# Kernel optimization log

Measured on AMD Instinct MI355X. Metric: run time of the kernel, lower is better.

The kernel has to match this reference:

```python
import jax, jax.numpy as jnp
import numpy as np

# Dims: B=batch, C=n_car, N=n_node, E=embed_dim, H=n_heads
B, C, N, E = 64, 8, 512, 512
H = 8
CLIP = 10.0


def setup_inputs() -> dict:
    key = jax.random.key(0)
    ks = jax.random.split(key, 12)
    s = 1.0 / np.sqrt(E)
    mask = jax.random.bernoulli(ks[10], 0.3, (B, C, 1, N))
    mask = mask.at[..., 0].set(False)  # ensure at least one unmasked node per (b,c)
    return {
        "node_embeddings": jax.random.normal(ks[0], (B, N, E), jnp.float32),
        "graph_embedding": jax.random.normal(ks[1], (B, E), jnp.float32),
        "step_context": jax.random.normal(ks[2], (B, C, 1, E + 2), jnp.float32),
        "mask": mask,
        "Wk1": jax.random.normal(ks[3], (E, E), jnp.float32) * s,
        "Wv": jax.random.normal(ks[4], (E, E), jnp.float32) * s,
        "Wk2": jax.random.normal(ks[5], (E, E), jnp.float32) * s,
        "Wq_fixed": jax.random.normal(ks[6], (E, E), jnp.float32) * s,
        "Wout": jax.random.normal(ks[7], (E, E), jnp.float32) * s,
        "Wq_step": jax.random.normal(ks[8], (E, E + 2), jnp.float32) * s,
        "v": jax.random.uniform(ks[9], (E,), jnp.float32, -s, s),
    }


def reference(node_embeddings, graph_embedding, step_context, mask,
              Wk1, Wv, Wk2, Wq_fixed, Wout, Wq_step, v):
    dh = E // H
    neg = jnp.asarray(-1e9, node_embeddings.dtype)

    # compute_static: projections (torch Linear: x @ W.T). K/V/Q_fixed are
    # broadcast over the car dim instead of materialized via .repeat (same math).
    Q_fixed = (graph_embedding @ Wq_fixed.T)[:, None, None, :]  # [B,1,1,E]
    K1 = node_embeddings @ Wk1.T                                 # [B,N,E]
    V = node_embeddings @ Wv.T                                   # [B,N,E]
    K2 = node_embeddings @ Wk2.T                                 # [B,N,E]

    # compute_dynamic
    Q_step = step_context @ Wq_step.T                            # [B,C,1,E]
    Q1 = Q_fixed + Q_step                                        # [B,C,1,E]

    # MHA (need_W=False): split heads, masked scaled dot-product, merge heads.
    qh = Q1.reshape(B, C, H, dh)                                 # q-len 1 squeezed
    kh = K1.reshape(B, N, H, dh)
    vh = V.reshape(B, N, H, dh)
    scores = jnp.einsum('bchd,bnhd->bchn', qh, kh) * (1.0 / np.sqrt(dh))
    m = mask[:, :, 0, :][:, :, None, :]                          # [B,C,1,N]
    scores = jnp.where(m, neg, scores)
    attn = jax.nn.softmax(scores, axis=-1)
    heads = jnp.einsum('bchn,bnhd->bchd', attn, vh).reshape(B, C, E)
    Q3 = heads @ Wout.T                                          # [B,C,E] (Q2.squeeze(2))

    # Pointer logits (SHA): u = tanh(Q_fixed+Q_step) @ v, repeated over E,
    # dotted with K2 => u_scalar * sum_e K2, then tanh-clipped and masked.
    u_scalar = jnp.einsum('bcqe,e->bcq', jnp.tanh(Q1), v)        # [B,C,1]
    k2sum = K2.sum(-1)                                           # [B,N]
    raw = u_scalar * k2sum[:, None, :]                           # [B,C,N]
    logits = CLIP * jnp.tanh(raw * (1.0 / np.sqrt(E)))
    logits = jnp.where(mask[:, :, 0, :], neg, logits)
    logits = logits.reshape(B, C * N)                            # view(batch, -1)
    return logits, Q3
```

## Files before the change

kernel.cpp:

```cpp
#include <hip/hip_runtime.h>


typedef _Float16 f16x8 __attribute__((ext_vector_type(8)));
typedef float f32x4 __attribute__((ext_vector_type(4)));

__device__ __forceinline__ void async16(const void* g, void* l) {
  __builtin_amdgcn_global_load_lds(
      (const __attribute__((address_space(1))) unsigned int*)g,
      (__attribute__((address_space(3))) unsigned int*)l, 16, 0, 0);
}

__global__ __launch_bounds__(256) void prep_w(const float* __restrict__ Wk1,
                                              const float* __restrict__ Wv,
                                              const float* __restrict__ Wk2,
                                              _Float16* __restrict__ W1h,
                                              _Float16* __restrict__ W2h,
                                              float* __restrict__ colsum) {
  const int bid = blockIdx.x;
  if (bid < 16) {
    const int tx = threadIdx.x & 31, ty = threadIdx.x >> 5;
    const int col = bid * 32 + tx;
    float s = 0.f;
#pragma unroll 4
    for (int e = ty * 64; e < ty * 64 + 64; ++e) s += Wk2[e * 512 + col];
    __shared__ float red[8][32];
    red[ty][tx] = s;
    __syncthreads();
    if (ty == 0) {
      float t = 0.f;
#pragma unroll
      for (int g = 0; g < 8; ++g) t += red[g][tx];
      colsum[col] = t;
    }
  } else {
    const int cb = bid - 16;
    const float* src = (cb < 128) ? Wk1 : Wv;
    _Float16* dst = (cb < 128) ? W1h : W2h;
    const size_t off = (size_t)(cb & 127) * 2048 + threadIdx.x * 8;
    float4 a = *(const float4*)(src + off);
    float4 b = *(const float4*)(src + off + 4);
    union { _Float16 h[8]; uint4 u; } pk;
    pk.h[0] = (_Float16)a.x; pk.h[1] = (_Float16)a.y;
    pk.h[2] = (_Float16)a.z; pk.h[3] = (_Float16)a.w;
    pk.h[4] = (_Float16)b.x; pk.h[5] = (_Float16)b.y;
    pk.h[6] = (_Float16)b.z; pk.h[7] = (_Float16)b.w;
    *(uint4*)(dst + off) = pk.u;
  }
}

__global__ __launch_bounds__(256) void q1_mfma_kernel(
    const float* __restrict__ ge, const float* __restrict__ sc,
    const float* __restrict__ Wqf, const float* __restrict__ Wqs,
    float* __restrict__ Q1) {
  const int mb = blockIdx.x, nb = blockIdx.y, ks = blockIdx.z;
  const int tid = threadIdx.x;
  const int lane = tid & 63, wave = tid >> 6;
  const int wm = (wave >> 1) * 32, wn = (wave & 1) * 32;

  __shared__ __align__(16) _Float16 As[64][40];
  __shared__ __align__(16) _Float16 Ws[64][40];

  f32x4 acc[2][2] = {};
  const int qd = (lane >> 4) * 8, rr = lane & 15;

  for (int kt = 0; kt < 9; ++kt) {
    const int kb = ks * 288 + kt * 32;
#pragma unroll
    for (int f0 = 0; f0 < 2; ++f0) {
      int f = tid + f0 * 256;
      int r = f >> 3, c4 = (f & 7) * 4;
      int m = mb * 64 + r;
      int e = nb * 64 + r;
#pragma unroll
      for (int j = 0; j < 4; ++j) {
        int k = kb + c4 + j;
        float a = 0.f, w = 0.f;
        if (k < 512) {
          a = ge[(m >> 3) * 512 + k];
          w = Wqf[(size_t)e * 512 + k];
        } else if (k < 1026) {
          a = sc[(size_t)m * 514 + (k - 512)];
          w = Wqs[(size_t)e * 514 + (k - 512)];
        }
        As[r][c4 + j] = (_Float16)a;
        Ws[r][c4 + j] = (_Float16)w;
      }
    }
    __syncthreads();
    f16x8 af[2], bfr[2];
#pragma unroll
    for (int mi = 0; mi < 2; ++mi) af[mi] = *(const f16x8*)&As[wm + mi * 16 + rr][qd];
#pragma unroll
    for (int ni = 0; ni < 2; ++ni) bfr[ni] = *(const f16x8*)&Ws[wn + ni * 16 + rr][qd];
#pragma unroll
    for (int mi = 0; mi < 2; ++mi)
#pragma unroll
      for (int ni = 0; ni < 2; ++ni)
        acc[mi][ni] =
            __builtin_amdgcn_mfma_f32_16x16x32_f16(af[mi], bfr[ni], acc[mi][ni], 0, 0, 0);
    __syncthreads();
  }

  const int col = lane & 15, rq = (lane >> 4) * 4;
#pragma unroll
  for (int mi = 0; mi < 2; ++mi)
#pragma unroll
    for (int ni = 0; ni < 2; ++ni)
#pragma unroll
      for (int r = 0; r < 4; ++r) {
        int m = mb * 64 + wm + mi * 16 + rq + r;
        int e = nb * 64 + wn + ni * 16 + col;
        atomicAdd(&Q1[(size_t)m * 512 + e], acc[mi][ni][r]);
      }
}

__global__ __launch_bounds__(256, 2) void gemm_kv(
    const float* __restrict__ A, const _Float16* __restrict__ W1,
    const _Float16* __restrict__ W2, const float* __restrict__ colsum,
    _Float16* __restrict__ K1, _Float16* __restrict__ Vt,
    float* __restrict__ k2sum) {
  const int nb = blockIdx.x;
  const int mb = blockIdx.y;
  const int tid = threadIdx.x, lane = tid & 63, wave = tid >> 6;
  const int wm = (wave >> 1) * 64, wn = (wave & 1) * 64;
  const int row0 = mb * 128, col0 = nb * 128;
  const int b = mb >> 2;

  __shared__ __align__(16) float Afs[128 * 64];
  __shared__ __align__(16) _Float16 Wbuf[2][128 * 64];

  f32x4 acc1[4][4] = {}, acc2[4][4] = {};
  float k2p = 0.f;
  const int q = lane >> 4, rr = lane & 15;
  const int wlr = lane >> 3, wlc = lane & 7;
  const int cswz = wlc ^ wlr;

  for (int kt = 0; kt < 8; ++kt) {
    const int kbase = kt * 64;
#pragma unroll
    for (int j = 0; j < 4; ++j) {
      int r = wave * 32 + j * 8 + wlr;
      int ldsrow = (wave * 32 + j * 8) * 64;
      size_t goff = (size_t)(col0 + r) * 512 + kbase + cswz * 8;
      async16(W1 + goff, &Wbuf[0][ldsrow]);
      async16(W2 + goff, &Wbuf[1][ldsrow]);
    }
#pragma unroll
    for (int j = 0; j < 8; ++j) {
      int r = wave * 32 + j * 4 + (lane >> 4);
      int cg = (lane & 15) ^ (r & 7);
      async16(A + (size_t)(row0 + r) * 512 + kbase + cg * 4,
              &Afs[(wave * 32 + j * 4) * 64]);
    }
    __syncthreads();
#pragma unroll
    for (int k0 = 0; k0 < 64; k0 += 32) {
      const int cb = (k0 >> 3) + q;
      const int ca = (k0 >> 2) + q * 2;
      f16x8 af[4], b1[4], b2[4];
#pragma unroll
      for (int mi = 0; mi < 4; ++mi) {
        int ra = wm + mi * 16 + rr;
        const float* base = &Afs[ra * 64];
        float4 lo = *(const float4*)(base + ((ca ^ (ra & 7)) * 4));
        float4 hi = *(const float4*)(base + (((ca + 1) ^ (ra & 7)) * 4));
        f16x8 v;
        v[0] = (_Float16)lo.x; v[1] = (_Float16)lo.y;
        v[2] = (_Float16)lo.z; v[3] = (_Float16)lo.w;
        v[4] = (_Float16)hi.x; v[5] = (_Float16)hi.y;
        v[6] = (_Float16)hi.z; v[7] = (_Float16)hi.w;
        af[mi] = v;
      }
#pragma unroll
      for (int ni = 0; ni < 4; ++ni) {
        int rw = wn + ni * 16 + rr;
        int slot = cb ^ (rw & 7);
        b1[ni] = *(const f16x8*)&Wbuf[0][rw * 64 + slot * 8];
        b2[ni] = *(const f16x8*)&Wbuf[1][rw * 64 + slot * 8];
      }
#pragma unroll
      for (int mi = 0; mi < 4; ++mi)
#pragma unroll
        for (int ni = 0; ni < 4; ++ni) {
          acc1[mi][ni] =
              __builtin_amdgcn_mfma_f32_16x16x32_f16(af[mi], b1[ni], acc1[mi][ni], 0, 0, 0);
          acc2[mi][ni] =
              __builtin_amdgcn_mfma_f32_16x16x32_f16(af[mi], b2[ni], acc2[mi][ni], 0, 0, 0);
        }
    }
    if (nb == 0) {
      int r = tid >> 1, cb0 = (tid & 1) * 8;
      const float* csp = colsum + kbase;
#pragma unroll
      for (int c = cb0; c < cb0 + 8; ++c) {
        int slot = c ^ (r & 7);
        float4 av = *(const float4*)&Afs[r * 64 + slot * 4];
        float4 cv = *(const float4*)(csp + c * 4);
        k2p += av.x * cv.x + av.y * cv.y + av.z * cv.z + av.w * cv.w;
      }
    }
    __syncthreads();
  }

  if (nb == 0) {
    k2p += __shfl_xor(k2p, 1, 64);
    if ((tid & 1) == 0) k2sum[row0 + (tid >> 1)] = k2p;
  }

  const int col = lane & 15, rq = (lane >> 4) * 4;
#pragma unroll
  for (int mi = 0; mi < 4; ++mi)
#pragma unroll
    for (int ni = 0; ni < 4; ++ni)
#pragma unroll
      for (int r = 0; r < 4; ++r) {
        size_t m = row0 + wm + mi * 16 + rq + r;
        size_t e = col0 + wn + ni * 16 + col;
        K1[m * 512 + e] = (_Float16)acc1[mi][ni][r];
      }

  _Float16* Vts = (_Float16*)&Afs[0];
#pragma unroll
  for (int mi = 0; mi < 4; ++mi)
#pragma unroll
    for (int ni = 0; ni < 4; ++ni) {
      int n0 = wm + mi * 16 + rq;
      int el = wn + ni * 16 + col;
      int cn = n0 >> 3, half = (n0 >> 2) & 1;
      int slot = cn ^ (el & 7);
      union { _Float16 h[4]; unsigned long long u; } pk;
#pragma unroll
      for (int r = 0; r < 4; ++r) pk.h[r] = (_Float16)acc2[mi][ni][r];
      *(unsigned long long*)&Vts[el * 128 + slot * 8 + half * 4] = pk.u;
    }
  __syncthreads();
  const int nbase = row0 & 511;
#pragma unroll
  for (int i = 0; i < 8; ++i) {
    int f = tid + i * 256;
    int el = f >> 4, c16 = f & 15;
    int slot = c16 ^ (el & 7);
    uint4 val = *(const uint4*)&Vts[el * 128 + slot * 8];
    *(uint4*)(Vt + (size_t)b * 262144 + (size_t)(col0 + el) * 512 + nbase + c16 * 8) = val;
  }
}

__global__ __launch_bounds__(256) void attn_kernel(
    const float* __restrict__ Q1, const _Float16* __restrict__ K1,
    const _Float16* __restrict__ Vt, const int* __restrict__ mask,
    float* __restrict__ heads) {
  const int bid = blockIdx.x;
  const int b = bid >> 3, h = bid & 7;
  const int tid = threadIdx.x, wave = tid >> 6, lane = tid & 63;
  const int q = lane >> 4, cl = lane & 15;

  __shared__ __align__(16) _Float16 kt[256 * 64];
  __shared__ __align__(16) _Float16 P[16][520];
  __shared__ float red[4][8];

  f16x8 af[2];
  {
    const float* qp = Q1 + (size_t)(b * 8 + (cl & 7)) * 512 + h * 64 + q * 8;
#pragma unroll
    for (int s = 0; s < 2; ++s) {
      float4 l0 = *(const float4*)(qp + s * 32);
      float4 l1 = *(const float4*)(qp + s * 32 + 4);
      af[s][0] = (_Float16)l0.x; af[s][1] = (_Float16)l0.y;
      af[s][2] = (_Float16)l0.z; af[s][3] = (_Float16)l0.w;
      af[s][4] = (_Float16)l1.x; af[s][5] = (_Float16)l1.y;
      af[s][6] = (_Float16)l1.z; af[s][7] = (_Float16)l1.w;
    }
  }

  f32x4 acc[8] = {};
  const _Float16* Kb = K1 + (size_t)b * 262144 + h * 64;
  for (int h2 = 0; h2 < 2; ++h2) {
#pragma unroll
    for (int j = 0; j < 8; ++j) {
      int r = wave * 64 + j * 8 + (lane >> 3);
      int cg = (lane & 7) ^ (r & 7);
      async16(Kb + (size_t)(h2 * 256 + r) * 512 + cg * 8, &kt[(wave * 64 + j * 8) * 64]);
    }
    __syncthreads();
#pragma unroll
    for (int tt = 0; tt < 4; ++tt) {
      int rn = wave * 64 + tt * 16 + cl;
#pragma unroll
      for (int s = 0; s < 2; ++s) {
        int slot = (s * 4 + q) ^ (cl & 7);
        f16x8 bf = *(const f16x8*)&kt[rn * 64 + slot * 8];
        acc[h2 * 4 + tt] =
            __builtin_amdgcn_mfma_f32_16x16x32_f16(af[s], bf, acc[h2 * 4 + tt], 0, 0, 0);
      }
    }
    __syncthreads();
  }

  const _Float16* Vb = Vt + (size_t)b * 262144 + (size_t)h * 64 * 512;
#pragma unroll
  for (int j = 0; j < 8; ++j) {
    int r = wave * 16 + j * 2 + (lane >> 5);
    int cg = (lane & 31) ^ (r & 7);
    async16(Vb + (size_t)r * 512 + cg * 8, &kt[(wave * 16 + j * 2) * 256]);
  }

  float gmax[4], rsum[4];
  if (q < 2) {
    float mx[4] = {-3e38f, -3e38f, -3e38f, -3e38f};
#pragma unroll
    for (int t = 0; t < 8; ++t) {
      int n = (t >> 2) * 256 + wave * 64 + (t & 3) * 16 + cl;
#pragma unroll
      for (int r = 0; r < 4; ++r) {
        int c = q * 4 + r;
        float x = mask[(size_t)(b * 8 + c) * 512 + n] ? -1e9f : acc[t][r] * 0.125f;
        acc[t][r] = x;
        mx[r] = fmaxf(mx[r], x);
      }
    }
#pragma unroll
    for (int off = 1; off < 16; off <<= 1)
#pragma unroll
      for (int r = 0; r < 4; ++r) mx[r] = fmaxf(mx[r], __shfl_xor(mx[r], off, 64));
    if (cl == 0)
#pragma unroll
      for (int r = 0; r < 4; ++r) red[wave][q * 4 + r] = mx[r];
  }
  __syncthreads();
  if (q < 2) {
#pragma unroll
    for (int r = 0; r < 4; ++r) {
      int c = q * 4 + r;
      gmax[r] = fmaxf(fmaxf(red[0][c], red[1][c]), fmaxf(red[2][c], red[3][c]));
    }
  }
  __syncthreads();
  if (q < 2) {
#pragma unroll
    for (int r = 0; r < 4; ++r) rsum[r] = 0.f;
#pragma unroll
    for (int t = 0; t < 8; ++t) {
      int n = (t >> 2) * 256 + wave * 64 + (t & 3) * 16 + cl;
#pragma unroll
      for (int r = 0; r < 4; ++r) {
        float e = __expf(acc[t][r] - gmax[r]);
        rsum[r] += e;
        P[q * 4 + r][n] = (_Float16)e;
      }
    }
#pragma unroll
    for (int off = 1; off < 16; off <<= 1)
#pragma unroll
      for (int r = 0; r < 4; ++r) rsum[r] += __shfl_xor(rsum[r], off, 64);
    if (cl == 0)
#pragma unroll
      for (int r = 0; r < 4; ++r) red[wave][q * 4 + r] = rsum[r];
  }
  __syncthreads();

  f32x4 pacc = {};
  const int rn = wave * 16 + cl;
#pragma unroll
  for (int sl = 0; sl < 8; ++sl) {
    int slot = (sl * 4 + q) ^ (cl & 7);
    f16x8 bf = *(const f16x8*)&kt[rn * 256 + slot * 8];
    f16x8 pa = *(const f16x8*)&P[cl][sl * 32 + q * 8];
    pacc = __builtin_amdgcn_mfma_f32_16x16x32_f16(pa, bf, pacc, 0, 0, 0);
  }
  __syncthreads();
#pragma unroll
  for (int j = 0; j < 8; ++j) {
    int r = wave * 16 + j * 2 + (lane >> 5);
    int cg = (lane & 31) ^ (r & 7);
    async16(Vb + (size_t)r * 512 + 256 + cg * 8, &kt[(wave * 16 + j * 2) * 256]);
  }
  __syncthreads();
#pragma unroll
  for (int sl = 0; sl < 8; ++sl) {
    int slot = (sl * 4 + q) ^ (cl & 7);
    f16x8 bf = *(const f16x8*)&kt[rn * 256 + slot * 8];
    f16x8 pa = *(const f16x8*)&P[cl][256 + sl * 32 + q * 8];
    pacc = __builtin_amdgcn_mfma_f32_16x16x32_f16(pa, bf, pacc, 0, 0, 0);
  }

  if (q < 2) {
#pragma unroll
    for (int r = 0; r < 4; ++r) {
      int c = q * 4 + r;
      float inv = 1.f / (red[0][c] + red[1][c] + red[2][c] + red[3][c]);
      heads[(size_t)(b * 8 + c) * 512 + h * 64 + wave * 16 + cl] = pacc[r] * inv;
    }
  }
}

__global__ __launch_bounds__(256) void gemm_out64(const float* __restrict__ A,
                                                  const float* __restrict__ W,
                                                  float* __restrict__ C) {
  const int mb = blockIdx.x, nb = blockIdx.y, ks = blockIdx.z;
  const int tid = threadIdx.x;
  const int lane = tid & 63, wave = tid >> 6;
  const int wm = (wave >> 1) * 32, wn = (wave & 1) * 32;

  __shared__ __align__(16) _Float16 As[64][40];
  __shared__ __align__(16) _Float16 Ws[64][40];

  f32x4 acc[2][2] = {};
  const int qd = (lane >> 4) * 8, rr = lane & 15;

  for (int kt = 0; kt < 8; ++kt) {
    const int kb = ks * 256 + kt * 32;
#pragma unroll
    for (int f0 = 0; f0 < 2; ++f0) {
      int f = tid + f0 * 256;
      int r = f >> 3, c4 = (f & 7) * 4;
      float4 a = *(const float4*)(A + (size_t)(mb * 64 + r) * 512 + kb + c4);
      float4 w = *(const float4*)(W + (size_t)(nb * 64 + r) * 512 + kb + c4);
      As[r][c4 + 0] = (_Float16)a.x; As[r][c4 + 1] = (_Float16)a.y;
      As[r][c4 + 2] = (_Float16)a.z; As[r][c4 + 3] = (_Float16)a.w;
      Ws[r][c4 + 0] = (_Float16)w.x; Ws[r][c4 + 1] = (_Float16)w.y;
      Ws[r][c4 + 2] = (_Float16)w.z; Ws[r][c4 + 3] = (_Float16)w.w;
    }
    __syncthreads();
    f16x8 af[2], bfr[2];
#pragma unroll
    for (int mi = 0; mi < 2; ++mi) af[mi] = *(const f16x8*)&As[wm + mi * 16 + rr][qd];
#pragma unroll
    for (int ni = 0; ni < 2; ++ni) bfr[ni] = *(const f16x8*)&Ws[wn + ni * 16 + rr][qd];
#pragma unroll
    for (int mi = 0; mi < 2; ++mi)
#pragma unroll
      for (int ni = 0; ni < 2; ++ni)
        acc[mi][ni] =
            __builtin_amdgcn_mfma_f32_16x16x32_f16(af[mi], bfr[ni], acc[mi][ni], 0, 0, 0);
    __syncthreads();
  }

  const int col = lane & 15, rq = (lane >> 4) * 4;
#pragma unroll
  for (int mi = 0; mi < 2; ++mi)
#pragma unroll
    for (int ni = 0; ni < 2; ++ni)
#pragma unroll
      for (int r = 0; r < 4; ++r) {
        int m = mb * 64 + wm + mi * 16 + rq + r;
        int e = nb * 64 + wn + ni * 16 + col;
        atomicAdd(&C[(size_t)m * 512 + e], acc[mi][ni][r]);
      }
}

__global__ __launch_bounds__(256) void logits_u_kernel(
    const float* __restrict__ Q1, const float* __restrict__ v,
    const float* __restrict__ k2s, const int* __restrict__ mask,
    float* __restrict__ out) {
  const int bc = blockIdx.x;
  const int b = bc >> 3;
  const int tid = threadIdx.x;
  const int wave = tid >> 6, lane = tid & 63;

  float p = tanhf(Q1[(size_t)bc * 512 + tid]) * v[tid] +
            tanhf(Q1[(size_t)bc * 512 + tid + 256]) * v[tid + 256];
#pragma unroll
  for (int off = 32; off; off >>= 1) p += __shfl_down(p, off, 64);
  __shared__ float red[4];
  __shared__ float su;
  if (lane == 0) red[wave] = p;
  __syncthreads();
  if (tid == 0) su = red[0] + red[1] + red[2] + red[3];
  __syncthreads();
  const float u = su;

#pragma unroll
  for (int i = 0; i < 2; ++i) {
    int n = tid + i * 256;
    int idx = bc * 512 + n;
    out[idx] = mask[idx] ? -1e9f
                         : 10.f * tanhf(u * k2s[b * 512 + n] * 0.04419417382415922f);
  }
}

extern "C" void kernel_launch(void* const* d_in, const int* in_sizes, int n_in,
                              void* d_out, int out_size, void* d_ws, size_t ws_size,
                              hipStream_t stream) {
  const float* ne = (const float*)d_in[0];
  const float* ge = (const float*)d_in[1];
  const float* sc = (const float*)d_in[2];
  const int* mask = (const int*)d_in[3];
  const float* Wk1 = (const float*)d_in[4];
  const float* Wv = (const float*)d_in[5];
  const float* Wk2 = (const float*)d_in[6];
  const float* Wqf = (const float*)d_in[7];
  const float* Wout = (const float*)d_in[8];
  const float* Wqs = (const float*)d_in[9];
  const float* v = (const float*)d_in[10];

  float* logits = (float*)d_out;
  float* q3 = (float*)d_out + 262144;

  char* ws = (char*)d_ws;
  _Float16* K1 = (_Float16*)(ws + 0);
  _Float16* Vt = (_Float16*)(ws + 33554432);
  float* Q1 = (float*)(ws + 67108864);
  float* heads = (float*)(ws + 68157440);
  float* k2sum = (float*)(ws + 69206016);
  float* colsum = (float*)(ws + 69337088);
  _Float16* W1h = (_Float16*)(ws + 69339136);
  _Float16* W2h = (_Float16*)(ws + 69863424);

  hipMemsetAsync(Q1, 0, 1048576, stream);
  hipMemsetAsync(q3, 0, 1048576, stream);
  prep_w<<<272, 256, 0, stream>>>(Wk1, Wv, Wk2, W1h, W2h, colsum);
  q1_mfma_kernel<<<dim3(8, 8, 4), 256, 0, stream>>>(ge, sc, Wqf, Wqs, Q1);
  gemm_kv<<<dim3(4, 256), 256, 0, stream>>>(ne, W1h, W2h, colsum, K1, Vt, k2sum);
  attn_kernel<<<512, 256, 0, stream>>>(Q1, K1, Vt, mask, heads);
  gemm_out64<<<dim3(8, 8, 2), 256, 0, stream>>>(heads, Wout, q3);
  logits_u_kernel<<<512, 256, 0, stream>>>(Q1, v, k2sum, mask, logits);
}
```

Before: 224.3 us.

## Double-buffer W tiles and prefetch A via registers with fp16 LDS staging

New measurement: 214.4 us. 1.05x faster.

```diff
diff --git a/kernel.cpp b/kernel.cpp
--- a/kernel.cpp
+++ b/kernel.cpp
@@ -126,57 +126,90 @@
   const int row0 = mb * 128, col0 = nb * 128;
   const int b = mb >> 2;
 
-  __shared__ __align__(16) float Afs[128 * 64];
-  __shared__ __align__(16) _Float16 Wbuf[2][128 * 64];
+  __shared__ __align__(16) _Float16 Ah[128 * 64];
+  __shared__ __align__(16) _Float16 Wb[2][2][128 * 64];
 
   f32x4 acc1[4][4] = {}, acc2[4][4] = {};
-  float k2p = 0.f;
+  float k2p[4] = {0.f, 0.f, 0.f, 0.f};
   const int q = lane >> 4, rr = lane & 15;
   const int wlr = lane >> 3, wlc = lane & 7;
   const int cswz = wlc ^ wlr;
 
-  for (int kt = 0; kt < 8; ++kt) {
+  const int ar0 = tid >> 3, ac = tid & 7;
+  const float* aptr = A + (size_t)(row0 + ar0) * 512 + ac * 8;
+  const int aslot = ac ^ (ar0 & 7);
+
+  float4 areg[4][2];
+
+  auto issue_a = [&](int kt) {
+#pragma unroll
+    for (int j = 0; j < 4; ++j) {
+      const float* gp = aptr + (size_t)j * 32 * 512 + kt * 64;
+      areg[j][0] = *(const float4*)gp;
+      areg[j][1] = *(const float4*)(gp + 4);
+    }
+  };
+  auto issue_w = [&](int kt, int buf) {
     const int kbase = kt * 64;
 #pragma unroll
     for (int j = 0; j < 4; ++j) {
       int r = wave * 32 + j * 8 + wlr;
       int ldsrow = (wave * 32 + j * 8) * 64;
       size_t goff = (size_t)(col0 + r) * 512 + kbase + cswz * 8;
-      async16(W1 + goff, &Wbuf[0][ldsrow]);
-      async16(W2 + goff, &Wbuf[1][ldsrow]);
-    }
-#pragma unroll
-    for (int j = 0; j < 8; ++j) {
-      int r = wave * 32 + j * 4 + (lane >> 4);
-      int cg = (lane & 15) ^ (r & 7);
-      async16(A + (size_t)(row0 + r) * 512 + kbase + cg * 4,
-              &Afs[(wave * 32 + j * 4) * 64]);
-    }
-    __syncthreads();
+      async16(W1 + goff, &Wb[buf][0][ldsrow]);
+      async16(W2 + goff, &Wb[buf][1][ldsrow]);
+    }
+  };
+  auto write_a = [&](int kt) {
+#pragma unroll
+    for (int j = 0; j < 4; ++j) {
+      union { _Float16 h[8]; uint4 u; } pk;
+      float4 lo = areg[j][0], hi = areg[j][1];
+      pk.h[0] = (_Float16)lo.x; pk.h[1] = (_Float16)lo.y;
+      pk.h[2] = (_Float16)lo.z; pk.h[3] = (_Float16)lo.w;
+      pk.h[4] = (_Float16)hi.x; pk.h[5] = (_Float16)hi.y;
+      pk.h[6] = (_Float16)hi.z; pk.h[7] = (_Float16)hi.w;
+      *(uint4*)&Ah[(ar0 + 32 * j) * 64 + aslot * 8] = pk.u;
+    }
+    if (nb == 0) {
+      const float* csp = colsum + kt * 64 + ac * 8;
+      float4 c0 = *(const float4*)csp;
+      float4 c1 = *(const float4*)(csp + 4);
+#pragma unroll
+      for (int j = 0; j < 4; ++j) {
+        float4 lo = areg[j][0], hi = areg[j][1];
+        k2p[j] += lo.x * c0.x + lo.y * c0.y + lo.z * c0.z + lo.w * c0.w +
+                  hi.x * c1.x + hi.y * c1.y + hi.z * c1.z + hi.w * c1.w;
+      }
+    }
+  };
+
+  issue_a(0);
+  issue_w(0, 0);
+  write_a(0);
+  __syncthreads();
+
+  for (int kt = 0; kt < 8; ++kt) {
+    const int p = kt & 1;
+    if (kt < 7) {
+      issue_a(kt + 1);
+      issue_w(kt + 1, p ^ 1);
+    }
 #pragma unroll
     for (int k0 = 0; k0 < 64; k0 += 32) {
       const int cb = (k0 >> 3) + q;
-      const int ca = (k0 >> 2) + q * 2;
       f16x8 af[4], b1[4], b2[4];
 #pragma unroll
       for (int mi = 0; mi < 4; ++mi) {
         int ra = wm + mi * 16 + rr;
-        const float* base = &Afs[ra * 64];
-        float4 lo = *(const float4*)(base + ((ca ^ (ra & 7)) * 4));
-        float4 hi = *(const float4*)(base + (((ca + 1) ^ (ra & 7)) * 4));
-        f16x8 v;
-        v[0] = (_Float16)lo.x; v[1] = (_Float16)lo.y;
-        v[2] = (_Float16)lo.z; v[3] = (_Float16)lo.w;
-        v[4] = (_Float16)hi.x; v[5] = (_Float16)hi.y;
-        v[6] = (_Float16)hi.z; v[7] = (_Float16)hi.w;
-        af[mi] = v;
+        af[mi] = *(const f16x8*)&Ah[ra * 64 + (cb ^ (ra & 7)) * 8];
       }
 #pragma unroll
       for (int ni = 0; ni < 4; ++ni) {
         int rw = wn + ni * 16 + rr;
         int slot = cb ^ (rw & 7);
-        b1[ni] = *(const f16x8*)&Wbuf[0][rw * 64 + slot * 8];
-        b2[ni] = *(const f16x8*)&Wbuf[1][rw * 64 + slot * 8];
+        b1[ni] = *(const f16x8*)&Wb[p][0][rw * 64 + slot * 8];
+        b2[ni] = *(const f16x8*)&Wb[p][1][rw * 64 + slot * 8];
       }
 #pragma unroll
       for (int mi = 0; mi < 4; ++mi)
@@ -188,23 +221,22 @@
               __builtin_amdgcn_mfma_f32_16x16x32_f16(af[mi], b2[ni], acc2[mi][ni], 0, 0, 0);
         }
     }
-    if (nb == 0) {
-      int r = tid >> 1, cb0 = (tid & 1) * 8;
-      const float* csp = colsum + kbase;
-#pragma unroll
-      for (int c = cb0; c < cb0 + 8; ++c) {
-        int slot = c ^ (r & 7);
-        float4 av = *(const float4*)&Afs[r * 64 + slot * 4];
-        float4 cv = *(const float4*)(csp + c * 4);
-        k2p += av.x * cv.x + av.y * cv.y + av.z * cv.z + av.w * cv.w;
-      }
-    }
-    __syncthreads();
+    if (kt < 7) {
+      __syncthreads();
+      write_a(kt + 1);
+      __syncthreads();
+    }
   }
 
   if (nb == 0) {
-    k2p += __shfl_xor(k2p, 1, 64);
-    if ((tid & 1) == 0) k2sum[row0 + (tid >> 1)] = k2p;
+#pragma unroll
+    for (int j = 0; j < 4; ++j) {
+      float s = k2p[j];
+      s += __shfl_xor(s, 1, 8);
+      s += __shfl_xor(s, 2, 8);
+      s += __shfl_xor(s, 4, 8);
+      if (ac == 0) k2sum[row0 + ar0 + 32 * j] = s;
+    }
   }
 
   const int col = lane & 15, rq = (lane >> 4) * 4;
@@ -219,7 +251,7 @@
         K1[m * 512 + e] = (_Float16)acc1[mi][ni][r];
       }
 
-  _Float16* Vts = (_Float16*)&Afs[0];
+  _Float16* Vts = &Wb[0][0][0];
 #pragma unroll
   for (int mi = 0; mi < 4; ++mi)
 #pragma unroll
```
